# Kernel optimization log

Hardware: AMD Instinct MI355X
Metric: run time of the kernel (lower is better)

## Reference

```python
import jax, jax.numpy as jnp
import numpy as np

N_NODES = 30  # module caps nodes at 30 per graph
D = 768       # legal-bert hidden size


def setup_inputs() -> dict:
    key = jax.random.key(0)
    k1, k2, k3 = jax.random.split(key, 3)
    B, S = 256, 512
    bert_out = jax.random.normal(k1, (B, S, D), dtype=jnp.float32)
    re_w = jax.random.normal(k2, (2 * D,), dtype=jnp.float32) * 0.02  # Linear(1536,1).weight flattened
    re_b = jax.random.normal(k3, (1,), dtype=jnp.float32)
    return {"bert_out": bert_out, "re_w": re_w, "re_b": re_b}


def reference(bert_out, re_w, re_b):
    # mode='re' branch: all-pairs entity relation scoring.
    # score(j,k) = sigmoid(W @ concat(e_j, e_k) + b)
    #            = sigmoid(w1 @ e_j + w2 @ e_k + b), w1 = W[:768], w2 = W[768:]
    E = bert_out[:, :N_NODES, :]                    # [B, n, D] entity embeds
    w1, w2 = re_w[:D], re_w[D:]
    s = jnp.einsum('bnd,d->bn', E, w1)              # [B, n] left-half projections
    t = jnp.einsum('bnd,d->bn', E, w2)              # [B, n] right-half projections
    iu, ju = np.triu_indices(N_NODES, k=1)          # static 435 upper-tri pairs
    scores = jax.nn.sigmoid(s[:, iu] + t[:, ju] + re_b[0])  # [B, 435]
    # torch.cat over graphs then squeeze(-1) -> flat [B*435]
    return scores.reshape(-1)
```

## Files before the change

kernel.cpp:

```cpp
#include <hip/hip_runtime.h>
#include <math.h>

#define N_NODES 30
#define DD 768
#define SS 512
#define NPAIRS 435

__global__ __launch_bounds__(512) void legal_pair_kernel(
    const float* __restrict__ bert,
    const float* __restrict__ re_w,
    const float* __restrict__ re_b,
    float* __restrict__ out)
{
    const int b    = blockIdx.x;
    const int tid  = threadIdx.x;
    const int lane = tid & 63;
    const int wave = tid >> 6;

    __shared__ float s_sm[N_NODES];
    __shared__ float t_sm[N_NODES];

    const float4* w1p = reinterpret_cast<const float4*>(re_w);
    const float4* w2p = reinterpret_cast<const float4*>(re_w + DD);
    float4 w1v[3], w2v[3];
    #pragma unroll
    for (int it = 0; it < 3; ++it) {
        w1v[it] = w1p[lane + 64 * it];
        w2v[it] = w2p[lane + 64 * it];
    }

    const float* Eb = bert + (size_t)b * SS * DD;

    for (int n = wave; n < N_NODES; n += 8) {
        const float4* row = reinterpret_cast<const float4*>(Eb + (size_t)n * DD);
        float s = 0.f, t = 0.f;
        #pragma unroll
        for (int it = 0; it < 3; ++it) {
            float4 e = row[lane + 64 * it];
            s += e.x * w1v[it].x + e.y * w1v[it].y + e.z * w1v[it].z + e.w * w1v[it].w;
            t += e.x * w2v[it].x + e.y * w2v[it].y + e.z * w2v[it].z + e.w * w2v[it].w;
        }
        #pragma unroll
        for (int off = 32; off > 0; off >>= 1) {
            s += __shfl_xor(s, off, 64);
            t += __shfl_xor(t, off, 64);
        }
        if (lane == 0) { s_sm[n] = s; t_sm[n] = t; }
    }
    __syncthreads();

    const float bias = re_b[0];
    if (tid < NPAIRS) {
        const int p = tid;
        int i = (int)((59.0f - sqrtf((float)(3481 - 8 * p))) * 0.5f);
        while (i * (59 - i) / 2 > p) --i;
        while ((i + 1) * (58 - i) / 2 <= p) ++i;
        const int j = p - i * (59 - i) / 2 + i + 1;
        const float x = s_sm[i] + t_sm[j] + bias;
        out[(size_t)b * NPAIRS + p] = 1.0f / (1.0f + expf(-x));
    }
}

extern "C" void kernel_launch(void* const* d_in, const int* in_sizes, int n_in,
                              void* d_out, int out_size, void* d_ws, size_t ws_size,
                              hipStream_t stream) {
    const float* bert = (const float*)d_in[0];
    const float* re_w = (const float*)d_in[1];
    const float* re_b = (const float*)d_in[2];
    float* out = (float*)d_out;

    const int B = in_sizes[0] / (SS * DD);
    legal_pair_kernel<<<B, 512, 0, stream>>>(bert, re_w, re_b, out);
}
```

Measured before the change: 9.780 us.

## Use 15 waves per block, each computing two entity rows with loads issued upfront

The block grows from 512 to 960 threads, so 15 wavefronts each handle exactly two of the 30 entity rows (wave and wave+15). Before, 8 waves looped over up to four rows each. All row and weight float4 loads are now issued before any arithmetic, so more global loads are in flight at once. The aim is to hide memory latency in this small, latency-bound kernel. In exchange, register pressure per thread rises, and the larger block has more threads idle in the final pair stage. Some unused leftover variables remain.

```diff
diff --git a/kernel.cpp b/kernel.cpp
--- a/kernel.cpp
+++ b/kernel.cpp
@@ -6,7 +6,7 @@
 #define SS 512
 #define NPAIRS 435
 
-__global__ __launch_bounds__(512) void legal_pair_kernel(
+__global__ __launch_bounds__(960) void legal_pair_kernel(
     const float* __restrict__ bert,
     const float* __restrict__ re_w,
     const float* __restrict__ re_b,
@@ -20,32 +20,46 @@
     __shared__ float s_sm[N_NODES];
     __shared__ float t_sm[N_NODES];
 
+    const float* Eb = bert + (size_t)b * SS * DD;
+    const int r0 = 2 * wave;
+    const int r1 = (wave < 15) ? 0 : 0;
+    (void)r1;
+
+    const int ra = wave;
+    const int rb = wave + 15;
+
     const float4* w1p = reinterpret_cast<const float4*>(re_w);
     const float4* w2p = reinterpret_cast<const float4*>(re_w + DD);
-    float4 w1v[3], w2v[3];
+    const float4* rowA = reinterpret_cast<const float4*>(Eb + (size_t)ra * DD);
+    const float4* rowB = reinterpret_cast<const float4*>(Eb + (size_t)rb * DD);
+
+    float4 w1v[3], w2v[3], eA[3], eB[3];
     #pragma unroll
     for (int it = 0; it < 3; ++it) {
+        eA[it]  = rowA[lane + 64 * it];
+        eB[it]  = rowB[lane + 64 * it];
         w1v[it] = w1p[lane + 64 * it];
         w2v[it] = w2p[lane + 64 * it];
     }
 
-    const float* Eb = bert + (size_t)b * SS * DD;
-
-    for (int n = wave; n < N_NODES; n += 8) {
-        const float4* row = reinterpret_cast<const float4*>(Eb + (size_t)n * DD);
-        float s = 0.f, t = 0.f;
-        #pragma unroll
-        for (int it = 0; it < 3; ++it) {
-            float4 e = row[lane + 64 * it];
-            s += e.x * w1v[it].x + e.y * w1v[it].y + e.z * w1v[it].z + e.w * w1v[it].w;
-            t += e.x * w2v[it].x + e.y * w2v[it].y + e.z * w2v[it].z + e.w * w2v[it].w;
-        }
-        #pragma unroll
-        for (int off = 32; off > 0; off >>= 1) {
-            s += __shfl_xor(s, off, 64);
-            t += __shfl_xor(t, off, 64);
-        }
-        if (lane == 0) { s_sm[n] = s; t_sm[n] = t; }
+    float sA = 0.f, tA = 0.f, sB = 0.f, tB = 0.f;
+    #pragma unroll
+    for (int it = 0; it < 3; ++it) {
+        sA += eA[it].x * w1v[it].x + eA[it].y * w1v[it].y + eA[it].z * w1v[it].z + eA[it].w * w1v[it].w;
+        tA += eA[it].x * w2v[it].x + eA[it].y * w2v[it].y + eA[it].z * w2v[it].z + eA[it].w * w2v[it].w;
+        sB += eB[it].x * w1v[it].x + eB[it].y * w1v[it].y + eB[it].z * w1v[it].z + eB[it].w * w1v[it].w;
+        tB += eB[it].x * w2v[it].x + eB[it].y * w2v[it].y + eB[it].z * w2v[it].z + eB[it].w * w2v[it].w;
+    }
+    #pragma unroll
+    for (int off = 32; off > 0; off >>= 1) {
+        sA += __shfl_xor(sA, off, 64);
+        tA += __shfl_xor(tA, off, 64);
+        sB += __shfl_xor(sB, off, 64);
+        tB += __shfl_xor(tB, off, 64);
+    }
+    if (lane == 0) {
+        s_sm[ra] = sA;  t_sm[ra] = tA;
+        s_sm[rb] = sB;  t_sm[rb] = tB;
     }
     __syncthreads();
 
@@ -70,5 +84,5 @@
     float* out = (float*)d_out;
 
     const int B = in_sizes[0] / (SS * DD);
-    legal_pair_kernel<<<B, 512, 0, stream>>>(bert, re_w, re_b, out);
+    legal_pair_kernel<<<B, 960, 0, stream>>>(bert, re_w, re_b, out);
 }
```

New measurement: 9.706 us. No clear change (-0.8%).
